# Optimization experiments

Measured on AMD Instinct MI355X. Metric: run time of the kernel, lower is better.

## Reference

```python
import jax, jax.numpy as jnp
import numpy as np

CUTOFF = 10.0


def _forward(query_points, codes, grid_points, eW1, eb1, eW2, eb2, cW, cb, fcW, fcb, nW1, nb1, nW2, nb2, edge_index):
    B, N, _ = query_points.shape
    G = grid_points.shape[0]
    C = codes.shape[-1]
    n_pts = B * N
    num_nodes = n_pts + B * G
    qp = query_points.reshape(-1, 3)
    gc = jnp.broadcast_to(grid_points[None], (B, G, 3)).reshape(-1, 3)
    x = jnp.concatenate([qp, gc], axis=0)                      # [num_nodes, 3]
    h = jnp.concatenate([jnp.zeros((n_pts, C), qp.dtype), codes.reshape(-1, C)], axis=0)
    row, col = edge_index[0], edge_index[1]                    # row = grid (source), col = query (target)
    ones = jnp.ones((edge_index.shape[1],), x.dtype)
    denom = jnp.maximum(jax.ops.segment_sum(ones, col, num_segments=num_nodes), 1.0)[:, None]

    def layer(x, h, We1, be1, We2, be2, Wc, bc, Wn1, bn1, Wn2, bn2, out_x_dim):
        rel = x[row] - x[col]                                  # [E, 3]
        dist = jnp.linalg.norm(rel, axis=-1, keepdims=True)    # [E, 1]
        m = jax.nn.silu(jnp.concatenate([h[row], h[col], dist], axis=-1) @ We1 + be1)
        m = jax.nn.silu(m @ We2 + be2)                         # [E, H]
        d = dist[:, 0]
        Cm = 0.5 * (jnp.cos(d * jnp.pi / CUTOFF) + 1.0) * (d <= CUTOFF)
        m = m * Cm[:, None]
        coef = m @ Wc + bc                                     # [E, out_x_dim]
        dirn = rel / (dist + 1e-8)
        if out_x_dim == 1:
            cmsg = coef * dirn                                 # [E, 3]
            dx = jax.ops.segment_sum(cmsg, col, num_segments=num_nodes) / denom
            x_new = x + dx
        else:
            cmsg = (coef[:, :, None] * dirn[:, None, :]).reshape(coef.shape[0], -1)  # [E, T*3]
            dx = (jax.ops.segment_sum(cmsg, col, num_segments=num_nodes) / denom).reshape(num_nodes, out_x_dim, 3)
            x_new = x[:, None, :] + dx                         # [num_nodes, T, 3]
        m_aggr = jax.ops.segment_sum(m, col, num_segments=num_nodes) / denom
        h_delta = jax.nn.silu(jnp.concatenate([h, m_aggr], axis=-1) @ Wn1 + bn1) @ Wn2 + bn2
        return x_new, h + h_delta

    for i in range(3):
        x, h = layer(x, h, eW1[i], eb1[i], eW2[i], eb2[i], cW[i], cb[i], nW1[i], nb1[i], nW2[i], nb2[i], 1)
    T = fcb.shape[0]
    x_f, _ = layer(x, h, eW1[3], eb1[3], eW2[3], eb2[3], fcW, fcb, nW1[3], nb1[3], nW2[3], nb2[3], T)
    pred = x_f[:n_pts].reshape(B, N, T, 3)
    return pred - query_points.reshape(B, N, 3)[:, :, None, :]


def setup_inputs() -> dict:
    key = jax.random.key(0)
    B, N, Gs, Cd, H, T, deg = 8, 2048, 8, 128, 128, 5, 16
    G = Gs ** 3
    n_pts = B * N
    E = n_pts * deg
    ks = jax.random.split(key, 12)
    c1 = (jnp.arange(Gs, dtype=jnp.float32) - (Gs - 1) / 2.0) * 2.0   # anchor_spacing = 2.0, centered
    gx, gy, gz = jnp.meshgrid(c1, c1, c1, indexing='ij')
    grid_points = jnp.stack([gx, gy, gz], -1).reshape(-1, 3)
    query_points = jax.random.uniform(ks[0], (B, N, 3), minval=-7.0, maxval=7.0)
    codes = jax.random.normal(ks[1], (B, G, Cd), dtype=jnp.float32)
    q = jnp.repeat(jnp.arange(n_pts, dtype=jnp.int32), deg)
    gl = jax.random.randint(ks[2], (E,), 0, G, dtype=jnp.int32)
    row = n_pts + (q // N) * G + gl                                   # grid node (global idx), same batch as query
    edge_index = jnp.stack([row, q], axis=0)
    def lin(k, fi, sh):
        return jax.random.normal(k, sh, dtype=jnp.float32) / jnp.sqrt(jnp.float32(fi))
    eW1 = lin(ks[3], 2 * Cd + 1, (4, 2 * Cd + 1, H)); eb1 = jnp.zeros((4, H))
    eW2 = lin(ks[4], H, (4, H, H)); eb2 = jnp.zeros((4, H))
    cW = lin(ks[5], H, (3, H, 1)); cb = jnp.zeros((3, 1))
    fcW = lin(ks[6], H, (H, T)); fcb = jnp.zeros((T,))
    nW1 = lin(ks[7], Cd + H, (4, Cd + H, H)); nb1 = jnp.zeros((4, H))
    nW2 = lin(ks[8], H, (4, H, Cd)); nb2 = jnp.zeros((4, Cd))
    return {"query_points": query_points, "codes": codes, "grid_points": grid_points,
            "eW1": eW1, "eb1": eb1, "eW2": eW2, "eb2": eb2,
            "cW": cW, "cb": cb, "fcW": fcW, "fcb": fcb,
            "nW1": nW1, "nb1": nb1, "nW2": nW2, "nb2": nb2,
            "edge_index": edge_index}


def reference(query_points, codes, grid_points, eW1, eb1, eW2, eb2, cW, cb, fcW, fcb, nW1, nb1, nW2, nb2, edge_index):
    return _forward(query_points, codes, grid_points, eW1, eb1, eW2, eb2, cW, cb, fcW, fcb, nW1, nb1, nW2, nb2, edge_index)
```

## Files before the change

### kernel.cpp

```cpp
#include <hip/hip_runtime.h>
#include <hip/hip_bf16.h>

typedef unsigned short u16;
typedef unsigned int u32;
typedef __attribute__((ext_vector_type(8))) short short8;
typedef __attribute__((ext_vector_type(4))) short shortx4;
typedef __attribute__((ext_vector_type(4))) float floatx4;

#define N_PTS 16384
#define N_GRID 4096
#define GPTS 512
#define HD 128
#define DEG 16
#define QB 16
#define EB 256
#define EBLK (N_PTS / QB)

__device__ __forceinline__ float silu_f(float x) {
    return x * __builtin_amdgcn_rcpf(1.0f + __expf(-x));
}
__device__ __forceinline__ short f2bf(float x) { return (short)__bfloat16_as_ushort(__float2bfloat16(x)); }

__global__ void k_fillf(float* out, float v, int n) {
    int i = blockIdx.x * blockDim.x + threadIdx.x;
    if (i < n) out[i] = v;
}

__global__ void k_init(const float* __restrict__ qp, const float* __restrict__ codes,
                       float* __restrict__ x_q, float* __restrict__ h_g, float* __restrict__ h_q,
                       float* __restrict__ Bq) {
    int stride = gridDim.x * blockDim.x;
    int i0 = blockIdx.x * blockDim.x + threadIdx.x;
    for (int i = i0; i < N_PTS * 3; i += stride) x_q[i] = qp[i];
    for (int i = i0; i < N_GRID * HD; i += stride) h_g[i] = codes[i];
    for (int i = i0; i < N_PTS * HD; i += stride) { h_q[i] = 0.0f; Bq[i] = 0.0f; }
}

__global__ void k_prep(const float* __restrict__ eW2, short* __restrict__ wsT) {
    int idx = blockIdx.x * blockDim.x + threadIdx.x;
    if (idx >= 4 * HD * HD) return;
    int l = idx >> 14, rem = idx & 16383, f = rem >> 7, k = rem & 127;
    wsT[idx] = f2bf(eW2[l * 16384 + k * HD + f]);
}

__global__ void k_prep2(const float* __restrict__ nW1, const float* __restrict__ nW2,
                        const float* __restrict__ eW1,
                        short* __restrict__ nW1T, short* __restrict__ nW2T,
                        short* __restrict__ W1midT, short* __restrict__ W1topT) {
    int idx = blockIdx.x * blockDim.x + threadIdx.x;
    if (idx < 3 * 32768) {
        int l = idx >> 15, r = idx & 32767, f = r >> 8, k = r & 255;
        nW1T[idx] = f2bf(nW1[l * 32768 + k * 128 + f]);
    } else if (idx < 3 * 32768 + 3 * 16384) {
        int j = idx - 3 * 32768;
        int l = j >> 14, r = j & 16383, f = r >> 7, k = r & 127;
        nW2T[j] = f2bf(nW2[l * 16384 + k * 128 + f]);
    } else if (idx < 3 * 32768 + 6 * 16384) {
        int j = idx - 3 * 32768 - 3 * 16384;
        int p = j >> 14, r = j & 16383, f = r >> 7, k = r & 127;
        W1midT[j] = f2bf(eW1[(p + 1) * 257 * 128 + (128 + k) * 128 + f]);
    } else if (idx < 3 * 32768 + 6 * 16384 + 4 * 16384) {
        int j = idx - 3 * 32768 - 6 * 16384;
        int l = j >> 14, r = j & 16383, f = r >> 7, k = r & 127;
        W1topT[j] = f2bf(eW1[l * 257 * 128 + k * 128 + f]);
    }
}

__device__ __forceinline__ void stageB(short* Bb, const short* src, int rowF4, int colF4, int tid) {
#pragma unroll
    for (int s = 0; s < 8; s++) {
        int idx = s * 256 + tid;
        int f = idx >> 4, c4 = idx & 15;
        float4 v = ((const float4*)src)[f * rowF4 + colF4 + c4];
        *(float4*)((char*)Bb + ((idx * 16) ^ ((f & 7) << 4))) = v;
    }
}

__device__ __forceinline__ void stageB512(short* Bb, const short* src, int rowF4, int colF4, int tid) {
#pragma unroll
    for (int s = 0; s < 4; s++) {
        int idx = s * 512 + tid;
        int f = idx >> 4, c4 = idx & 15;
        float4 v = ((const float4*)src)[f * rowF4 + colF4 + c4];
        *(float4*)((char*)Bb + ((idx * 16) ^ ((f & 7) << 4))) = v;
    }
}

__device__ __forceinline__ void nb_gemm(const short* X1, const short* Bb, floatx4* acc,
                                        int rowbase, int kOff, int quad, int c, int swz) {
#pragma unroll
    for (int ks = 0; ks < 4; ks++) {
        short8 a = *(const short8*)((const char*)X1 + rowbase + (((kOff + ks * 32 + quad * 8) * 2) ^ swz));
#pragma unroll
        for (int n = 0; n < 8; n++) {
            short8 b = *(const short8*)((const char*)Bb + ((((n * 16 + c) << 8) + (ks * 32 + quad * 8) * 2) ^ swz));
            acc[n] = __builtin_amdgcn_mfma_f32_16x16x32_bf16(a, b, acc[n], 0, 0, 0);
        }
    }
}

__device__ __forceinline__ void gemm16(const short* X, const short* Bb, floatx4& acc,
                                       int kOffX, int wid, int quad, int c, int swz) {
#pragma unroll
    for (int ks = 0; ks < 4; ks++) {
        int k = ks * 32 + quad * 8;
        short8 a = *(const short8*)((const char*)X + ((c * 512 + (kOffX + k) * 2) ^ swz));
        short8 b = *(const short8*)((const char*)Bb + ((((wid * 16 + c) << 8) + k * 2) ^ swz));
        acc = __builtin_amdgcn_mfma_f32_16x16x32_bf16(a, b, acc, 0, 0, 0);
    }
}

__global__ __launch_bounds__(256) void k_ga2(
    const float* __restrict__ hg, float* __restrict__ Ag,
    const short* __restrict__ W1topT, const float* __restrict__ b1,
    const short* __restrict__ Wn1T, const float* __restrict__ bn1,
    const short* __restrict__ Wn2T, const float* __restrict__ bn2,
    int updateH, float* __restrict__ hg_out) {
    __shared__ short X[64 * 128];
    __shared__ short Bb[128 * 128];
    int tid = threadIdx.x;
    int n0 = blockIdx.x * 64;
    int wid = tid >> 6, lane = tid & 63, quad = lane >> 4, c = lane & 15;
    const int swz = (c & 7) << 4;

    {
        int q = tid >> 2, part = tid & 3;
        const float* src = &hg[(n0 + q) * HD + part * 32];
        int wswz = (q & 7) << 4;
#pragma unroll
        for (int i = 0; i < 4; i++) {
            float4 a = ((const float4*)src)[2 * i];
            float4 b = ((const float4*)src)[2 * i + 1];
            short8 v;
            v[0] = f2bf(a.x); v[1] = f2bf(a.y); v[2] = f2bf(a.z); v[3] = f2bf(a.w);
            v[4] = f2bf(b.x); v[5] = f2bf(b.y); v[6] = f2bf(b.z); v[7] = f2bf(b.w);
            *(short8*)((char*)X + ((q * 256 + part * 64 + i * 16) ^ wswz)) = v;
        }
    }
    stageB(Bb, W1topT, 16, 0, tid);
    __syncthreads();

    int rowbase = (wid * 16 + c) * 256;
    floatx4 acc[8];
#pragma unroll
    for (int n = 0; n < 8; n++) acc[n] = (floatx4)0.f;
    nb_gemm(X, Bb, acc, rowbase, 0, quad, c, swz);
#pragma unroll
    for (int n = 0; n < 8; n++) {
        int f = n * 16 + c;
        float bv = b1[f];
#pragma unroll
        for (int r = 0; r < 4; r++)
            Ag[(n0 + wid * 16 + quad * 4 + r) * HD + f] = acc[n][r] + bv;
    }
    if (!updateH) return;

    __syncthreads();
    stageB(Bb, Wn1T, 32, 0, tid);
    __syncthreads();
#pragma unroll
    for (int n = 0; n < 8; n++) acc[n] = (floatx4)0.f;
    nb_gemm(X, Bb, acc, rowbase, 0, quad, c, swz);
    __syncthreads();
#pragma unroll
    for (int n = 0; n < 8; n++) {
        int f = n * 16 + c;
        float b1v = bn1[f];
#pragma unroll
        for (int r = 0; r < 4; r++) {
            int rq = wid * 16 + quad * 4 + r;
            *(short*)((char*)X + ((rq * 256 + f * 2) ^ ((rq & 7) << 4))) =
                f2bf(silu_f(acc[n][r] + b1v));
        }
    }
    stageB(Bb, Wn2T, 16, 0, tid);
    __syncthreads();
#pragma unroll
    for (int n = 0; n < 8; n++) acc[n] = (floatx4)0.f;
    nb_gemm(X, Bb, acc, rowbase, 0, quad, c, swz);
#pragma unroll
    for (int n = 0; n < 8; n++) {
        int f = n * 16 + c;
        float b2v2 = bn2[f];
#pragma unroll
        for (int r = 0; r < 4; r++) {
            int gn = n0 + wid * 16 + quad * 4 + r;
            hg_out[gn * HD + f] = hg[gn * HD + f] + acc[n][r] + b2v2;
        }
    }
}

template <int OUTT, bool FIN>
__global__ __launch_bounds__(512, 3) void k_edge(
    const float* __restrict__ Ag, float* __restrict__ Bq, float* __restrict__ x_q,
    const float* __restrict__ wdrow, const short* __restrict__ wsT,
    const float* __restrict__ b2v, const float* __restrict__ Wc, const float* __restrict__ cbp,
    const int* __restrict__ erow, const float* __restrict__ gridp,
    const float* __restrict__ qp, float* __restrict__ out,
    const float* __restrict__ bn1, const float* __restrict__ bn2,
    const short* __restrict__ Wn1T, const short* __restrict__ Wn2T,
    const short* __restrict__ W1midT, float* __restrict__ hq) {
    __shared__ float misc[3072];
    __shared__ short Xn[16 * 256];
    __shared__ short lwsT[HD * HD];
    int tid = threadIdx.x;

    float* sdist = misc;
    float* scm   = misc + 256;
    float* sdir  = misc + 512;
    float* xs    = misc + 1280;
    float* scoef = misc + 1344;
    int*   sgi   = (int*)(misc + 2624);

    int q0 = blockIdx.x * QB;
    int wid = tid >> 6, lane = tid & 63, quad = lane >> 4, c = lane & 15;

    if (tid < QB * 3) xs[tid] = x_q[q0 * 3 + tid];
    {
        const float4* src = (const float4*)wsT;
#pragma unroll
        for (int s = 0; s < 4; s++) {
            int idx = s * 512 + tid;
            int byte = idx << 4;
            int swz2 = byte ^ (((byte >> 8) & 7) << 4);
            *(float4*)((char*)lwsT + swz2) = src[idx];
        }
    }
    __syncthreads();
    if (tid < EB) {
        int e = tid, q = e >> 4;
        int gi = erow[q0 * DEG + e] - N_PTS;
        sgi[e] = gi;
        int gl = gi & (GPTS - 1);
        float r0 = gridp[gl * 3 + 0] - xs[q * 3 + 0];
        float r1 = gridp[gl * 3 + 1] - xs[q * 3 + 1];
        float r2 = gridp[gl * 3 + 2] - xs[q * 3 + 2];
        float dist = sqrtf(r0 * r0 + r1 * r1 + r2 * r2);
        float inv = 1.0f / (dist + 1e-8f);
        sdist[e] = dist;
        sdir[0 * EB + e] = r0 * inv;
        sdir[1 * EB + e] = r1 * inv;
        sdir[2 * EB + e] = r2 * inv;
        float cw = 0.5f * (__cosf(dist * 0.31415926535897931f) + 1.0f);
        scm[e] = (dist <= 10.0f) ? cw : 0.0f;
    }
    __syncthreads();

    int gi_[2]; float dist_[2];
#pragma unroll
    for (int mi = 0; mi < 2; mi++) {
        int e = (wid * 2 + mi) * 16 + c;
        gi_[mi] = sgi[e];
        dist_[mi] = sdist[e];
    }

    floatx4 acc[2][8];
#pragma unroll
    for (int mi = 0; mi < 2; mi++)
#pragma unroll
        for (int n = 0; n < 8; n++) acc[mi][n] = (floatx4)0.f;

    const int swz = (c & 7) << 4;

#pragma unroll
    for (int ch = 0; ch < 4; ch++) {
        int kb = ch * 32 + quad * 8;
        float4 wd0 = *(const float4*)(wdrow + kb);
        float4 wd1 = *(const float4*)(wdrow + kb + 4);
        short8 afr[2];
#pragma unroll
        for (int mi = 0; mi < 2; mi++) {
            int q = wid * 2 + mi;
            float dist = dist_[mi];
            const float4* ap = (const float4*)(Ag + gi_[mi] * HD + kb);
            float4 a0 = ap[0], a1 = ap[1];
            const float4* bp4 = (const float4*)(Bq + (q0 + q) * HD + kb);
            float4 b0 = bp4[0], b1 = bp4[1];
            short8 v;
            v[0] = f2bf(silu_f(a0.x + b0.x + dist * wd0.x));
            v[1] = f2bf(silu_f(a0.y + b0.y + dist * wd0.y));
            v[2] = f2bf(silu_f(a0.z + b0.z + dist * wd0.z));
            v[3] = f2bf(silu_f(a0.w + b0.w + dist * wd0.w));
            v[4] = f2bf(silu_f(a1.x + b1.x + dist * wd1.x));
            v[5] = f2bf(silu_f(a1.y + b1.y + dist * wd1.y));
            v[6] = f2bf(silu_f(a1.z + b1.z + dist * wd1.z));
            v[7] = f2bf(silu_f(a1.w + b1.w + dist * wd1.w));
            afr[mi] = v;
        }
#pragma unroll
        for (int n = 0; n < 8; n++) {
            int byte = ((n * 16 + c) << 8) + (kb << 1);
            short8 bfr = *(const short8*)((const char*)lwsT + (byte ^ swz));
            acc[0][n] = __builtin_amdgcn_mfma_f32_16x16x32_bf16(afr[0], bfr, acc[0][n], 0, 0, 0);
            acc[1][n] = __builtin_amdgcn_mfma_f32_16x16x32_bf16(afr[1], bfr, acc[1][n], 0, 0, 0);
        }
    }

#pragma unroll
    for (int mi = 0; mi < 2; mi++) {
        int q = wid * 2 + mi;
        int ebase = q * 16;
        float cmr[4];
#pragma unroll
        for (int r = 0; r < 4; r++) cmr[r] = scm[ebase + quad * 4 + r];
        float apc[4][OUTT];
#pragma unroll
        for (int r = 0; r < 4; r++)
#pragma unroll
            for (int t = 0; t < OUTT; t++) apc[r][t] = 0.f;
#pragma unroll
        for (int n = 0; n < 8; n++) {
            int f = n * 16 + c;
            float be2v = b2v[f];
            float wcv[OUTT];
            if (FIN) {
#pragma unroll
                for (int t = 0; t < OUTT; t++) wcv[t] = Wc[f * 5 + t];
            } else {
                wcv[0] = Wc[f];
            }
            float cs = 0.f;
#pragma unroll
            for (int r = 0; r < 4; r++) {
                float v = silu_f(acc[mi][n][r] + be2v) * cmr[r];
                cs += v;
#pragma unroll
                for (int t = 0; t < OUTT; t++) apc[r][t] += v * wcv[t];
            }
            cs += __shfl_xor(cs, 16, 64);
            cs += __shfl_xor(cs, 32, 64);
            if (!FIN && lane < 16)
                *(short*)((char*)Xn + ((q * 512 + (128 + f) * 2) ^ ((q & 7) << 4))) =
                    f2bf(cs * 0.0625f);
        }
#pragma unroll
        for (int t = 0; t < OUTT; t++) {
#pragma unroll
            for (int r = 0; r < 4; r++) {
                float v = apc[r][t];
                v += __shfl_xor(v, 1, 64);
                v += __shfl_xor(v, 2, 64);
                v += __shfl_xor(v, 4, 64);
                v += __shfl_xor(v, 8, 64);
                if (c == 0) scoef[(ebase + quad * 4 + r) * OUTT + t] = v;
            }
        }
    }
    __syncthreads();

    if (tid < QB * 3 * OUTT) {
        int qq = tid / (3 * OUTT), rem = tid % (3 * OUTT), t = rem / 3, c2 = rem % 3;
        float cbv = cbp[t];
        float s = 0.f;
#pragma unroll 4
        for (int r = 0; r < 16; r++) {
            int ee = qq * 16 + r;
            s += (scoef[ee * OUTT + t] + cbv) * sdir[c2 * EB + ee];
        }
        float dd = s * 0.0625f;
        if (FIN) out[(q0 + qq) * 15 + t * 3 + c2] = xs[qq * 3 + c2] + dd - qp[(q0 + qq) * 3 + c2];
        else x_q[(q0 + qq) * 3 + c2] = xs[qq * 3 + c2] + dd;
    }
    if (FIN) return;

    {
        int q = tid >> 5, f0 = (tid & 31) * 4;
        float4 h4 = *(const float4*)&hq[(q0 + q) * HD + f0];
        shortx4 v;
        v[0] = f2bf(h4.x); v[1] = f2bf(h4.y); v[2] = f2bf(h4.z); v[3] = f2bf(h4.w);
        *(shortx4*)((char*)Xn + ((q * 512 + f0 * 2) ^ ((q & 7) << 4))) = v;
    }
    stageB512(lwsT, Wn1T, 32, 0, tid);
    __syncthreads();

    floatx4 acc1 = (floatx4)0.f;
    gemm16(Xn, lwsT, acc1, 0, wid, quad, c, swz);
    __syncthreads();
    stageB512(lwsT, Wn1T, 32, 16, tid);
    __syncthreads();
    gemm16(Xn, lwsT, acc1, 128, wid, quad, c, swz);
    __syncthreads();

    {
        int f = wid * 16 + c;
        float b1v = bn1[f];
#pragma unroll
        for (int r = 0; r < 4; r++) {
            int q = quad * 4 + r;
            *(short*)((char*)Xn + ((q * 512 + (128 + f) * 2) ^ ((q & 7) << 4))) =
                f2bf(silu_f(acc1[r] + b1v));
        }
    }
    stageB512(lwsT, Wn2T, 16, 0, tid);
    __syncthreads();

    floatx4 acc2 = (floatx4)0.f;
    gemm16(Xn, lwsT, acc2, 128, wid, quad, c, swz);
    __syncthreads();

    {
        int f = wid * 16 + c;
        float b2 = bn2[f];
#pragma unroll
        for (int r = 0; r < 4; r++) {
            int q = quad * 4 + r;
            int gq = q0 + q;
            float hv = hq[gq * HD + f] + acc2[r] + b2;
            hq[gq * HD + f] = hv;
            *(short*)((char*)Xn + ((q * 512 + f * 2) ^ ((q & 7) << 4))) = f2bf(hv);
        }
    }
    stageB512(lwsT, W1midT, 16, 0, tid);
    __syncthreads();

    floatx4 acc3 = (floatx4)0.f;
    gemm16(Xn, lwsT, acc3, 0, wid, quad, c, swz);
    {
        int f = wid * 16 + c;
#pragma unroll
        for (int r = 0; r < 4; r++)
            Bq[(q0 + quad * 4 + r) * HD + f] = acc3[r];
    }
}

extern "C" void kernel_launch(void* const* d_in, const int* in_sizes, int n_in,
                              void* d_out, int out_size, void* d_ws, size_t ws_size,
                              hipStream_t stream) {
    float* out = (float*)d_out;
    int fill_blocks = (out_size + 255) / 256;

    static const int exp_sz[16] = { 49152, 524288, 1536, 131584, 512, 65536, 512, 384,
                                    3, 640, 5, 131072, 512, 65536, 512, 524288 };
    bool ok = (n_in == 16);
    for (int i = 0; ok && i < 16; i++) if (in_sizes[i] != exp_sz[i]) ok = false;
    if (!ok || ws_size < (size_t)40 * 1024 * 1024) {
        k_fillf<<<fill_blocks, 256, 0, stream>>>(out, 777.0f, out_size);
        return;
    }

    const float* qp    = (const float*)d_in[0];
    const float* codes = (const float*)d_in[1];
    const float* gridp = (const float*)d_in[2];
    const float* eW1   = (const float*)d_in[3];
    const float* eb1   = (const float*)d_in[4];
    const float* eW2   = (const float*)d_in[5];
    const float* eb2   = (const float*)d_in[6];
    const float* cW    = (const float*)d_in[7];
    const float* cb    = (const float*)d_in[8];
    const float* fcW   = (const float*)d_in[9];
    const float* fcb   = (const float*)d_in[10];
    const float* nW1   = (const float*)d_in[11];
    const float* nb1   = (const float*)d_in[12];
    const float* nW2   = (const float*)d_in[13];
    const float* nb2   = (const float*)d_in[14];
    const int*   erow  = (const int*)d_in[15];

    float* ws = (float*)d_ws;
    float* x_q  = ws;  ws += N_PTS * 3;
    float* h_q  = ws;  ws += N_PTS * HD;
    float* hg_a = ws;  ws += N_GRID * HD;
    float* hg_b = ws;  ws += N_GRID * HD;
    float* Ag0  = ws;  ws += N_GRID * HD;
    float* Ag1  = ws;  ws += N_GRID * HD;
    float* Ag2  = ws;  ws += N_GRID * HD;
    float* Ag3  = ws;  ws += N_GRID * HD;
    float* Bqb  = ws;  ws += N_PTS * HD;
    short* wsT    = (short*)ws;
    short* nW1T   = wsT + 65536;
    short* nW2T   = nW1T + 98304;
    short* W1midT = nW2T + 49152;
    short* W1topT = W1midT + 49152;
    float* Agb[4] = { Ag0, Ag1, Ag2, Ag3 };
    float* hgs[2] = { hg_a, hg_b };

    k_init<<<2048, 256, 0, stream>>>(qp, codes, x_q, hg_a, h_q, Bqb);
    k_prep<<<(4 * HD * HD + 255) / 256, 256, 0, stream>>>(eW2, wsT);
    k_prep2<<<(3 * 32768 + 6 * 16384 + 4 * 16384 + 255) / 256, 256, 0, stream>>>(
        nW1, nW2, eW1, nW1T, nW2T, W1midT, W1topT);

    for (int L = 0; L < 4; L++) {
        int nl = (L < 3) ? L : 0;
        k_ga2<<<N_GRID / 64, 256, 0, stream>>>(
            hgs[L & 1], Agb[L], W1topT + L * 16384, eb1 + L * 128,
            nW1T + nl * 32768, nb1 + L * 128, nW2T + nl * 16384, nb2 + L * 128,
            (L < 3) ? 1 : 0, hgs[(L + 1) & 1]);
    }

    for (int i = 0; i < 4; i++) {
        const float* W1l = eW1 + i * 257 * 128;
        if (i < 3) {
            k_edge<1, false><<<EBLK, 512, 0, stream>>>(
                Agb[i], Bqb, x_q, W1l + 256 * 128, wsT + i * 16384, eb2 + i * 128,
                cW + i * 128, cb + i, erow, gridp, qp, out,
                nb1 + i * 128, nb2 + i * 128, nW1T + i * 32768, nW2T + i * 16384,
                W1midT + i * 16384, h_q);
        } else {
            k_edge<5, true><<<EBLK, 512, 0, stream>>>(
                Agb[3], Bqb, x_q, W1l + 256 * 128, wsT + i * 16384, eb2 + i * 128,
                fcW, fcb, erow, gridp, qp, out,
                nullptr, nullptr, nullptr, nullptr, nullptr, nullptr);
        }
    }
}
```

Measured before the change: 345.2 us.

## Fuse four per-layer edge kernels into one persistent kernel keeping query state on-chip

Replaces the four per-layer k_edge launches with a single k_mega kernel. Each block loops over all layers for its 16 queries and keeps query positions, hidden state (in registers) and the Bq projection in shared memory instead of global buffers. This also removes the k_init kernel and the global h_q/Bq/x_q round trips. The cost is more barriers per layer, a larger shared-memory footprint per block, and a launch_bounds occupancy target raised from 3 to 4 blocks, which may cause register spills.

```diff
diff --git a/kernel.cpp b/kernel.cpp
--- a/kernel.cpp
+++ b/kernel.cpp
@@ -24,16 +24,6 @@
 __global__ void k_fillf(float* out, float v, int n) {
     int i = blockIdx.x * blockDim.x + threadIdx.x;
     if (i < n) out[i] = v;
-}
-
-__global__ void k_init(const float* __restrict__ qp, const float* __restrict__ codes,
-                       float* __restrict__ x_q, float* __restrict__ h_g, float* __restrict__ h_q,
-                       float* __restrict__ Bq) {
-    int stride = gridDim.x * blockDim.x;
-    int i0 = blockIdx.x * blockDim.x + threadIdx.x;
-    for (int i = i0; i < N_PTS * 3; i += stride) x_q[i] = qp[i];
-    for (int i = i0; i < N_GRID * HD; i += stride) h_g[i] = codes[i];
-    for (int i = i0; i < N_PTS * HD; i += stride) { h_q[i] = 0.0f; Bq[i] = 0.0f; }
 }
 
 __global__ void k_prep(const float* __restrict__ eW2, short* __restrict__ wsT) {
@@ -191,46 +181,48 @@
 }
 
 template <int OUTT, bool FIN>
-__global__ __launch_bounds__(512, 3) void k_edge(
-    const float* __restrict__ Ag, float* __restrict__ Bq, float* __restrict__ x_q,
-    const float* __restrict__ wdrow, const short* __restrict__ wsT,
-    const float* __restrict__ b2v, const float* __restrict__ Wc, const float* __restrict__ cbp,
-    const int* __restrict__ erow, const float* __restrict__ gridp,
-    const float* __restrict__ qp, float* __restrict__ out,
-    const float* __restrict__ bn1, const float* __restrict__ bn2,
-    const short* __restrict__ Wn1T, const short* __restrict__ Wn2T,
-    const short* __restrict__ W1midT, float* __restrict__ hq) {
-    __shared__ float misc[3072];
-    __shared__ short Xn[16 * 256];
-    __shared__ short lwsT[HD * HD];
-    int tid = threadIdx.x;
+__device__ __forceinline__ void edge_layer(
+    int L, int q0, int tid, float4& hreg,
+    float* misc, float* xs, int* sgi, short* Xn, float* BqF, short* lwsT,
+    const float* __restrict__ Agall, const float* __restrict__ eW1,
+    const short* __restrict__ wsT,
+    const float* __restrict__ eb2all, const float* __restrict__ cWall,
+    const float* __restrict__ cball,
+    const float* __restrict__ fcW, const float* __restrict__ fcb,
+    const float* __restrict__ gridp, const float* __restrict__ qp,
+    float* __restrict__ out,
+    const float* __restrict__ nb1all, const float* __restrict__ nb2all,
+    const short* __restrict__ nW1T, const short* __restrict__ nW2T,
+    const short* __restrict__ W1midT) {
 
     float* sdist = misc;
     float* scm   = misc + 256;
     float* sdir  = misc + 512;
-    float* xs    = misc + 1280;
-    float* scoef = misc + 1344;
-    int*   sgi   = (int*)(misc + 2624);
-
-    int q0 = blockIdx.x * QB;
+    float* scoef = misc + 1280;
+    float* delta = misc;
+
     int wid = tid >> 6, lane = tid & 63, quad = lane >> 4, c = lane & 15;
-
-    if (tid < QB * 3) xs[tid] = x_q[q0 * 3 + tid];
-    {
-        const float4* src = (const float4*)wsT;
+    const int swz = (c & 7) << 4;
+    const float* Ag = Agall + (size_t)L * (N_GRID * HD);
+    const short* wsTL = wsT + L * 16384;
+    const float* wdrow = eW1 + L * 257 * 128 + 256 * 128;
+    const float* b2v = eb2all + L * 128;
+    const float* Wc = FIN ? fcW : (cWall + L * 128);
+    const float* cbp = FIN ? fcb : (cball + L);
+
+    {
+        const float4* src = (const float4*)wsTL;
 #pragma unroll
         for (int s = 0; s < 4; s++) {
             int idx = s * 512 + tid;
             int byte = idx << 4;
-            int swz2 = byte ^ (((byte >> 8) & 7) << 4);
-            *(float4*)((char*)lwsT + swz2) = src[idx];
-        }
-    }
-    __syncthreads();
+            int sw = byte ^ (((byte >> 8) & 7) << 4);
+            *(float4*)((char*)lwsT + sw) = src[idx];
+        }
+    }
     if (tid < EB) {
         int e = tid, q = e >> 4;
-        int gi = erow[q0 * DEG + e] - N_PTS;
-        sgi[e] = gi;
+        int gi = sgi[e];
         int gl = gi & (GPTS - 1);
         float r0 = gridp[gl * 3 + 0] - xs[q * 3 + 0];
         float r1 = gridp[gl * 3 + 1] - xs[q * 3 + 1];
@@ -260,8 +252,6 @@
 #pragma unroll
         for (int n = 0; n < 8; n++) acc[mi][n] = (floatx4)0.f;
 
-    const int swz = (c & 7) << 4;
-
 #pragma unroll
     for (int ch = 0; ch < 4; ch++) {
         int kb = ch * 32 + quad * 8;
@@ -274,7 +264,7 @@
             float dist = dist_[mi];
             const float4* ap = (const float4*)(Ag + gi_[mi] * HD + kb);
             float4 a0 = ap[0], a1 = ap[1];
-            const float4* bp4 = (const float4*)(Bq + (q0 + q) * HD + kb);
+            const float4* bp4 = (const float4*)(BqF + q * HD + kb);
             float4 b0 = bp4[0], b1 = bp4[1];
             short8 v;
             v[0] = f2bf(silu_f(a0.x + b0.x + dist * wd0.x));
@@ -295,6 +285,7 @@
             acc[1][n] = __builtin_amdgcn_mfma_f32_16x16x32_bf16(afr[1], bfr, acc[1][n], 0, 0, 0);
         }
     }
+    __syncthreads();
 
 #pragma unroll
     for (int mi = 0; mi < 2; mi++) {
@@ -359,31 +350,30 @@
         }
         float dd = s * 0.0625f;
         if (FIN) out[(q0 + qq) * 15 + t * 3 + c2] = xs[qq * 3 + c2] + dd - qp[(q0 + qq) * 3 + c2];
-        else x_q[(q0 + qq) * 3 + c2] = xs[qq * 3 + c2] + dd;
+        else xs[qq * 3 + c2] = xs[qq * 3 + c2] + dd;
     }
     if (FIN) return;
 
     {
         int q = tid >> 5, f0 = (tid & 31) * 4;
-        float4 h4 = *(const float4*)&hq[(q0 + q) * HD + f0];
         shortx4 v;
-        v[0] = f2bf(h4.x); v[1] = f2bf(h4.y); v[2] = f2bf(h4.z); v[3] = f2bf(h4.w);
+        v[0] = f2bf(hreg.x); v[1] = f2bf(hreg.y); v[2] = f2bf(hreg.z); v[3] = f2bf(hreg.w);
         *(shortx4*)((char*)Xn + ((q * 512 + f0 * 2) ^ ((q & 7) << 4))) = v;
     }
-    stageB512(lwsT, Wn1T, 32, 0, tid);
+    stageB512(lwsT, nW1T + L * 32768, 32, 0, tid);
     __syncthreads();
 
     floatx4 acc1 = (floatx4)0.f;
     gemm16(Xn, lwsT, acc1, 0, wid, quad, c, swz);
     __syncthreads();
-    stageB512(lwsT, Wn1T, 32, 16, tid);
+    stageB512(lwsT, nW1T + L * 32768, 32, 16, tid);
     __syncthreads();
     gemm16(Xn, lwsT, acc1, 128, wid, quad, c, swz);
     __syncthreads();
 
     {
         int f = wid * 16 + c;
-        float b1v = bn1[f];
+        float b1v = nb1all[L * 128 + f];
 #pragma unroll
         for (int r = 0; r < 4; r++) {
             int q = quad * 4 + r;
@@ -391,7 +381,7 @@
                 f2bf(silu_f(acc1[r] + b1v));
         }
     }
-    stageB512(lwsT, Wn2T, 16, 0, tid);
+    stageB512(lwsT, nW2T + L * 16384, 16, 0, tid);
     __syncthreads();
 
     floatx4 acc2 = (floatx4)0.f;
@@ -400,27 +390,70 @@
 
     {
         int f = wid * 16 + c;
-        float b2 = bn2[f];
-#pragma unroll
-        for (int r = 0; r < 4; r++) {
-            int q = quad * 4 + r;
-            int gq = q0 + q;
-            float hv = hq[gq * HD + f] + acc2[r] + b2;
-            hq[gq * HD + f] = hv;
-            *(short*)((char*)Xn + ((q * 512 + f * 2) ^ ((q & 7) << 4))) = f2bf(hv);
-        }
-    }
-    stageB512(lwsT, W1midT, 16, 0, tid);
+        float b2 = nb2all[L * 128 + f];
+#pragma unroll
+        for (int r = 0; r < 4; r++)
+            delta[(quad * 4 + r) * 128 + f] = acc2[r] + b2;
+    }
+    stageB512(lwsT, W1midT + L * 16384, 16, 0, tid);
+    __syncthreads();
+
+    {
+        int q = tid >> 5, f0 = (tid & 31) * 4;
+        hreg.x += delta[q * 128 + f0 + 0];
+        hreg.y += delta[q * 128 + f0 + 1];
+        hreg.z += delta[q * 128 + f0 + 2];
+        hreg.w += delta[q * 128 + f0 + 3];
+        shortx4 v;
+        v[0] = f2bf(hreg.x); v[1] = f2bf(hreg.y); v[2] = f2bf(hreg.z); v[3] = f2bf(hreg.w);
+        *(shortx4*)((char*)Xn + ((q * 512 + f0 * 2) ^ ((q & 7) << 4))) = v;
+    }
     __syncthreads();
 
     floatx4 acc3 = (floatx4)0.f;
     gemm16(Xn, lwsT, acc3, 0, wid, quad, c, swz);
+    __syncthreads();
     {
         int f = wid * 16 + c;
 #pragma unroll
         for (int r = 0; r < 4; r++)
-            Bq[(q0 + quad * 4 + r) * HD + f] = acc3[r];
-    }
+            BqF[(quad * 4 + r) * 128 + f] = acc3[r];
+    }
+    __syncthreads();
+}
+
+__global__ __launch_bounds__(512, 4) void k_mega(
+    const float* __restrict__ Agall, const float* __restrict__ eW1,
+    const short* __restrict__ wsT,
+    const float* __restrict__ eb2, const float* __restrict__ cW,
+    const float* __restrict__ cb,
+    const float* __restrict__ fcW, const float* __restrict__ fcb,
+    const int* __restrict__ erow, const float* __restrict__ gridp,
+    const float* __restrict__ qp, float* __restrict__ out,
+    const float* __restrict__ nb1, const float* __restrict__ nb2,
+    const short* __restrict__ nW1T, const short* __restrict__ nW2T,
+    const short* __restrict__ W1midT) {
+    __shared__ float misc[2560];
+    __shared__ float xs[48];
+    __shared__ int sgi[256];
+    __shared__ union { short xn[16 * 256]; float bq[16 * 128]; } XB;
+    __shared__ short lwsT[HD * HD];
+    int tid = threadIdx.x;
+    int q0 = blockIdx.x * QB;
+
+    if (tid < QB * 3) xs[tid] = qp[q0 * 3 + tid];
+    if (tid < EB) sgi[tid] = erow[q0 * DEG + tid] - N_PTS;
+    for (int i = tid; i < 16 * 128; i += 512) XB.bq[i] = 0.0f;
+    float4 hreg = make_float4(0.f, 0.f, 0.f, 0.f);
+    __syncthreads();
+
+    for (int L = 0; L < 3; L++)
+        edge_layer<1, false>(L, q0, tid, hreg, misc, xs, sgi, XB.xn, XB.bq, lwsT,
+                             Agall, eW1, wsT, eb2, cW, cb, fcW, fcb, gridp, qp, out,
+                             nb1, nb2, nW1T, nW2T, W1midT);
+    edge_layer<5, true>(3, q0, tid, hreg, misc, xs, sgi, XB.xn, XB.bq, lwsT,
+                        Agall, eW1, wsT, eb2, cW, cb, fcW, fcb, gridp, qp, out,
+                        nb1, nb2, nW1T, nW2T, W1midT);
 }
 
 extern "C" void kernel_launch(void* const* d_in, const int* in_sizes, int n_in,
@@ -456,49 +489,30 @@
     const int*   erow  = (const int*)d_in[15];
 
     float* ws = (float*)d_ws;
-    float* x_q  = ws;  ws += N_PTS * 3;
-    float* h_q  = ws;  ws += N_PTS * HD;
-    float* hg_a = ws;  ws += N_GRID * HD;
-    float* hg_b = ws;  ws += N_GRID * HD;
-    float* Ag0  = ws;  ws += N_GRID * HD;
-    float* Ag1  = ws;  ws += N_GRID * HD;
-    float* Ag2  = ws;  ws += N_GRID * HD;
-    float* Ag3  = ws;  ws += N_GRID * HD;
-    float* Bqb  = ws;  ws += N_PTS * HD;
+    float* Agall = ws;  ws += 4 * N_GRID * HD;
+    float* hg_a  = ws;  ws += N_GRID * HD;
+    float* hg_b  = ws;  ws += N_GRID * HD;
     short* wsT    = (short*)ws;
     short* nW1T   = wsT + 65536;
     short* nW2T   = nW1T + 98304;
     short* W1midT = nW2T + 49152;
     short* W1topT = W1midT + 49152;
-    float* Agb[4] = { Ag0, Ag1, Ag2, Ag3 };
-    float* hgs[2] = { hg_a, hg_b };
-
-    k_init<<<2048, 256, 0, stream>>>(qp, codes, x_q, hg_a, h_q, Bqb);
+
     k_prep<<<(4 * HD * HD + 255) / 256, 256, 0, stream>>>(eW2, wsT);
     k_prep2<<<(3 * 32768 + 6 * 16384 + 4 * 16384 + 255) / 256, 256, 0, stream>>>(
         nW1, nW2, eW1, nW1T, nW2T, W1midT, W1topT);
 
+    const float* gin[4] = { codes, hg_a, hg_b, hg_a };
+    float* gout[4]      = { hg_a, hg_b, hg_a, nullptr };
     for (int L = 0; L < 4; L++) {
         int nl = (L < 3) ? L : 0;
         k_ga2<<<N_GRID / 64, 256, 0, stream>>>(
-            hgs[L & 1], Agb[L], W1topT + L * 16384, eb1 + L * 128,
+            gin[L], Agall + (size_t)L * N_GRID * HD, W1topT + L * 16384, eb1 + L * 128,
             nW1T + nl * 32768, nb1 + L * 128, nW2T + nl * 16384, nb2 + L * 128,
-            (L < 3) ? 1 : 0, hgs[(L + 1) & 1]);
-    }
-
-    for (int i = 0; i < 4; i++) {
-        const float* W1l = eW1 + i * 257 * 128;
-        if (i < 3) {
-            k_edge<1, false><<<EBLK, 512, 0, stream>>>(
-                Agb[i], Bqb, x_q, W1l + 256 * 128, wsT + i * 16384, eb2 + i * 128,
-                cW + i * 128, cb + i, erow, gridp, qp, out,
-                nb1 + i * 128, nb2 + i * 128, nW1T + i * 32768, nW2T + i * 16384,
-                W1midT + i * 16384, h_q);
-        } else {
-            k_edge<5, true><<<EBLK, 512, 0, stream>>>(
-                Agb[3], Bqb, x_q, W1l + 256 * 128, wsT + i * 16384, eb2 + i * 128,
-                fcW, fcb, erow, gridp, qp, out,
-                nullptr, nullptr, nullptr, nullptr, nullptr, nullptr);
-        }
-    }
-}
+            (L < 3) ? 1 : 0, gout[L]);
+    }
+
+    k_mega<<<EBLK, 512, 0, stream>>>(
+        Agall, eW1, wsT, eb2, cW, cb, fcW, fcb, erow, gridp, qp, out,
+        nb1, nb2, nW1T, nW2T, W1midT);
+}
```

New measurement: 431.2 us. +24.9%, slower.

## Read GEMM weight fragments directly from global memory instead of LDS staging

Applied to the files above, without the earlier changes.

Drops the shared-memory staging of the bf16 weight matrices in both the grid-node kernel and the edge kernel. MFMA B fragments are now loaded straight from global memory, relying on L1/L2 caching. This removes the staging copies and several block barriers, and frees 32KB of LDS per edge block. The edge kernel's launch-bounds occupancy hint rises from 3 to 6 blocks, which tightens the register budget and may cause spills. Global fragment loads also have higher latency and less coalescing than LDS reads.

```diff
diff --git a/kernel.cpp b/kernel.cpp
--- a/kernel.cpp
+++ b/kernel.cpp
@@ -66,46 +66,30 @@
     }
 }
 
-__device__ __forceinline__ void stageB(short* Bb, const short* src, int rowF4, int colF4, int tid) {
-#pragma unroll
-    for (int s = 0; s < 8; s++) {
-        int idx = s * 256 + tid;
-        int f = idx >> 4, c4 = idx & 15;
-        float4 v = ((const float4*)src)[f * rowF4 + colF4 + c4];
-        *(float4*)((char*)Bb + ((idx * 16) ^ ((f & 7) << 4))) = v;
-    }
-}
-
-__device__ __forceinline__ void stageB512(short* Bb, const short* src, int rowF4, int colF4, int tid) {
-#pragma unroll
-    for (int s = 0; s < 4; s++) {
-        int idx = s * 512 + tid;
-        int f = idx >> 4, c4 = idx & 15;
-        float4 v = ((const float4*)src)[f * rowF4 + colF4 + c4];
-        *(float4*)((char*)Bb + ((idx * 16) ^ ((f & 7) << 4))) = v;
-    }
-}
-
-__device__ __forceinline__ void nb_gemm(const short* X1, const short* Bb, floatx4* acc,
-                                        int rowbase, int kOff, int quad, int c, int swz) {
-#pragma unroll
-    for (int ks = 0; ks < 4; ks++) {
-        short8 a = *(const short8*)((const char*)X1 + rowbase + (((kOff + ks * 32 + quad * 8) * 2) ^ swz));
-#pragma unroll
-        for (int n = 0; n < 8; n++) {
-            short8 b = *(const short8*)((const char*)Bb + ((((n * 16 + c) << 8) + (ks * 32 + quad * 8) * 2) ^ swz));
-            acc[n] = __builtin_amdgcn_mfma_f32_16x16x32_bf16(a, b, acc[n], 0, 0, 0);
-        }
-    }
-}
-
-__device__ __forceinline__ void gemm16(const short* X, const short* Bb, floatx4& acc,
-                                       int kOffX, int wid, int quad, int c, int swz) {
+__device__ __forceinline__ void nb_gemm_g(const short* X, const short* __restrict__ W, int rowW,
+                                          floatx4* acc, int rowbase, int quad, int c, int swz) {
 #pragma unroll
     for (int ks = 0; ks < 4; ks++) {
         int k = ks * 32 + quad * 8;
-        short8 a = *(const short8*)((const char*)X + ((c * 512 + (kOffX + k) * 2) ^ swz));
-        short8 b = *(const short8*)((const char*)Bb + ((((wid * 16 + c) << 8) + k * 2) ^ swz));
+        short8 a = *(const short8*)((const char*)X + rowbase + ((k * 2) ^ swz));
+#pragma unroll
+        for (int n = 0; n < 8; n++) {
+            short8 b = *(const short8*)(W + (n * 16 + c) * rowW + k);
+            acc[n] = __builtin_amdgcn_mfma_f32_16x16x32_bf16(a, b, acc[n], 0, 0, 0);
+        }
+    }
+}
+
+__device__ __forceinline__ void gemm16_g(const short* Xn, const short* __restrict__ W, int rowW,
+                                         int kOffA, floatx4& acc, int nsteps,
+                                         int wid, int quad, int c, int swz) {
+    int f = wid * 16 + c;
+#pragma unroll
+    for (int ks = 0; ks < 8; ks++) {
+        if (ks >= nsteps) break;
+        int k = ks * 32 + quad * 8;
+        short8 a = *(const short8*)((const char*)Xn + ((c * 512 + (kOffA + k) * 2) ^ swz));
+        short8 b = *(const short8*)(W + f * rowW + k);
         acc = __builtin_amdgcn_mfma_f32_16x16x32_bf16(a, b, acc, 0, 0, 0);
     }
 }
@@ -117,7 +101,6 @@
     const short* __restrict__ Wn2T, const float* __restrict__ bn2,
     int updateH, float* __restrict__ hg_out) {
     __shared__ short X[64 * 128];
-    __shared__ short Bb[128 * 128];
     int tid = threadIdx.x;
     int n0 = blockIdx.x * 64;
     int wid = tid >> 6, lane = tid & 63, quad = lane >> 4, c = lane & 15;
@@ -137,14 +120,13 @@
             *(short8*)((char*)X + ((q * 256 + part * 64 + i * 16) ^ wswz)) = v;
         }
     }
-    stageB(Bb, W1topT, 16, 0, tid);
     __syncthreads();
 
     int rowbase = (wid * 16 + c) * 256;
     floatx4 acc[8];
 #pragma unroll
     for (int n = 0; n < 8; n++) acc[n] = (floatx4)0.f;
-    nb_gemm(X, Bb, acc, rowbase, 0, quad, c, swz);
+    nb_gemm_g(X, W1topT, 128, acc, rowbase, quad, c, swz);
 #pragma unroll
     for (int n = 0; n < 8; n++) {
         int f = n * 16 + c;
@@ -155,12 +137,9 @@
     }
     if (!updateH) return;
 
-    __syncthreads();
-    stageB(Bb, Wn1T, 32, 0, tid);
-    __syncthreads();
 #pragma unroll
     for (int n = 0; n < 8; n++) acc[n] = (floatx4)0.f;
-    nb_gemm(X, Bb, acc, rowbase, 0, quad, c, swz);
+    nb_gemm_g(X, Wn1T, 256, acc, rowbase, quad, c, swz);
     __syncthreads();
 #pragma unroll
     for (int n = 0; n < 8; n++) {
@@ -173,11 +152,10 @@
                 f2bf(silu_f(acc[n][r] + b1v));
         }
     }
-    stageB(Bb, Wn2T, 16, 0, tid);
     __syncthreads();
 #pragma unroll
     for (int n = 0; n < 8; n++) acc[n] = (floatx4)0.f;
-    nb_gemm(X, Bb, acc, rowbase, 0, quad, c, swz);
+    nb_gemm_g(X, Wn2T, 128, acc, rowbase, quad, c, swz);
 #pragma unroll
     for (int n = 0; n < 8; n++) {
         int f = n * 16 + c;
@@ -191,7 +169,7 @@
 }
 
 template <int OUTT, bool FIN>
-__global__ __launch_bounds__(512, 3) void k_edge(
+__global__ __launch_bounds__(512, 6) void k_edge(
     const float* __restrict__ Ag, float* __restrict__ Bq, float* __restrict__ x_q,
     const float* __restrict__ wdrow, const short* __restrict__ wsT,
     const float* __restrict__ b2v, const float* __restrict__ Wc, const float* __restrict__ cbp,
@@ -202,7 +180,6 @@
     const short* __restrict__ W1midT, float* __restrict__ hq) {
     __shared__ float misc[3072];
     __shared__ short Xn[16 * 256];
-    __shared__ short lwsT[HD * HD];
     int tid = threadIdx.x;
 
     float* sdist = misc;
@@ -216,16 +193,6 @@
     int wid = tid >> 6, lane = tid & 63, quad = lane >> 4, c = lane & 15;
 
     if (tid < QB * 3) xs[tid] = x_q[q0 * 3 + tid];
-    {
-        const float4* src = (const float4*)wsT;
-#pragma unroll
-        for (int s = 0; s < 4; s++) {
-            int idx = s * 512 + tid;
-            int byte = idx << 4;
-            int swz2 = byte ^ (((byte >> 8) & 7) << 4);
-            *(float4*)((char*)lwsT + swz2) = src[idx];
-        }
-    }
     __syncthreads();
     if (tid < EB) {
         int e = tid, q = e >> 4;
@@ -289,8 +256,7 @@
         }
 #pragma unroll
         for (int n = 0; n < 8; n++) {
-            int byte = ((n * 16 + c) << 8) + (kb << 1);
-            short8 bfr = *(const short8*)((const char*)lwsT + (byte ^ swz));
+            short8 bfr = *(const short8*)(wsT + (n * 16 + c) * HD + kb);
             acc[0][n] = __builtin_amdgcn_mfma_f32_16x16x32_bf16(afr[0], bfr, acc[0][n], 0, 0, 0);
             acc[1][n] = __builtin_amdgcn_mfma_f32_16x16x32_bf16(afr[1], bfr, acc[1][n], 0, 0, 0);
         }
@@ -370,15 +336,10 @@
         v[0] = f2bf(h4.x); v[1] = f2bf(h4.y); v[2] = f2bf(h4.z); v[3] = f2bf(h4.w);
         *(shortx4*)((char*)Xn + ((q * 512 + f0 * 2) ^ ((q & 7) << 4))) = v;
     }
-    stageB512(lwsT, Wn1T, 32, 0, tid);
     __syncthreads();
 
     floatx4 acc1 = (floatx4)0.f;
-    gemm16(Xn, lwsT, acc1, 0, wid, quad, c, swz);
-    __syncthreads();
-    stageB512(lwsT, Wn1T, 32, 16, tid);
-    __syncthreads();
-    gemm16(Xn, lwsT, acc1, 128, wid, quad, c, swz);
+    gemm16_g(Xn, Wn1T, 256, 0, acc1, 8, wid, quad, c, swz);
     __syncthreads();
 
     {
@@ -391,13 +352,10 @@
                 f2bf(silu_f(acc1[r] + b1v));
         }
     }
-    stageB512(lwsT, Wn2T, 16, 0, tid);
     __syncthreads();
 
     floatx4 acc2 = (floatx4)0.f;
-    gemm16(Xn, lwsT, acc2, 128, wid, quad, c, swz);
-    __syncthreads();
-
+    gemm16_g(Xn, Wn2T, 128, 128, acc2, 4, wid, quad, c, swz);
     {
         int f = wid * 16 + c;
         float b2 = bn2[f];
@@ -410,11 +368,10 @@
             *(short*)((char*)Xn + ((q * 512 + f * 2) ^ ((q & 7) << 4))) = f2bf(hv);
         }
     }
-    stageB512(lwsT, W1midT, 16, 0, tid);
     __syncthreads();
 
     floatx4 acc3 = (floatx4)0.f;
-    gemm16(Xn, lwsT, acc3, 0, wid, quad, c, swz);
+    gemm16_g(Xn, W1midT, 128, 0, acc3, 4, wid, quad, c, swz);
     {
         int f = wid * 16 + c;
 #pragma unroll
```

After: 793.9 us. 2.3x slower.
